# Kernel optimization log

Hardware: AMD Instinct MI355X
Metric: run time of the kernel (lower is better)

Reference implementation:

```python
import jax, jax.numpy as jnp
from jax import lax
import numpy as np

# HH / synapse constants (CFG in original repo; standard values matching the rate eqns)
GNA, GK, GL = 40.0, 35.0, 0.3
ENA, EK, EL = 55.0, -77.0, -65.0
GS, VS = 1.0, 0.0
IAPP = 1.0
VT, KP = -20.0, 3.0
A_D, A_R = 1.0, 0.1
DT = 0.02

B, N, L = 16, 2000, 1024


def setup_inputs() -> dict:
    key = jax.random.key(0)
    z = jax.random.uniform(key, (B, N, L), dtype=jnp.float32)
    return {"z": z}


def _rates(V):
    # Singularity-safe rate constants (the torch code patches V==25 / V==-35 exactly).
    at25 = V == 25.0
    atm35 = V == -35.0
    dN = jnp.where(at25, 1.0, 1.0 - jnp.exp((-V + 25.0) / 9.0))
    dM = jnp.where(atm35, 1.0, 1.0 - jnp.exp((-V - 35.0) / 9.0))
    dNb = jnp.where(at25, 1.0, 1.0 - jnp.exp((V - 25.0) / 9.0))
    dMb = jnp.where(atm35, 1.0, 1.0 - jnp.exp((V + 35.0) / 9.0))
    aN = jnp.where(at25, 0.18, 0.02 * (V - 25.0) / dN)
    bN = jnp.where(at25, 0.08, -0.002 * (V - 25.0) / dNb)
    aM = jnp.where(atm35, 1.638, 0.182 * (V + 35.0) / dM)
    bM = jnp.where(atm35, 1.16, -0.124 * (V + 35.0) / dMb)
    aH = 0.25 * jnp.exp((-V - 90.0) / 12.0)
    bH = 0.25 * jnp.exp((V + 34.0) / 12.0)
    return aN, bN, aM, bM, aH, bH


def _step(carry, z_prev):
    V, m, n, h, y = carry
    pow1 = GNA * m ** 3 * h
    pow2 = GK * n ** 4
    G = DT / 2 * (pow1 + pow2 + GL + GS * y)
    E = pow1 * ENA + pow2 * EK + GL * EL + GS * VS * y
    Vn = (V * (1.0 - G) + DT * (E + IAPP)) / (1.0 + G)
    aN, bN, aM, bM, aH, bH = _rates(Vn)
    mn = (aM * DT + (1.0 - DT / 2 * (aM + bM)) * m) / (DT / 2 * (aM + bM) + 1.0)
    nn = (aN * DT + (1.0 - DT / 2 * (aN + bN)) * n) / (DT / 2 * (aN + bN) + 1.0)
    hn = (aH * DT + (1.0 - DT / 2 * (aH + bH)) * h) / (DT / 2 * (aH + bH) + 1.0)
    ady = A_D * z_prev
    yn = (ady * DT + (1.0 - DT / 2 * (ady + A_R)) * y) / (DT / 2 * (ady + A_R) + 1.0)
    return (Vn, mn, nn, hn, yn), Vn


def _hh(z):
    b, n_t, l = z.shape
    zt = jnp.moveaxis(z, 1, 0)  # (N, B, L); step k uses z[k-1]
    V0 = jnp.full((b, l), -70.0, dtype=z.dtype)
    zeros = jnp.zeros((b, l), dtype=z.dtype)
    ones = jnp.ones((b, l), dtype=z.dtype)
    carry0 = (V0, zeros, zeros, ones, zeros)
    _, Vseq = lax.scan(_step, carry0, zt[:-1])  # (N-1, B, L)
    Vall = jnp.concatenate([V0[None], Vseq], axis=0)  # (N, B, L)
    V = jnp.moveaxis(Vall, 0, 1)  # (B, N, L)
    return jax.nn.sigmoid((V - VT) / KP)


def reference(z):
    return _hh(z)
```

## Files before the change

### kernel.cpp

```cpp
#include <hip/hip_runtime.h>

#define N_ 2000
#define L_ 1024

__device__ __forceinline__ float rcpf(float d) { return __builtin_amdgcn_rcpf(d); }
__device__ __forceinline__ float ex2(float x)  { return __builtin_amdgcn_exp2f(x); }

#define STEP2(K, RS, DOSTORE)                                                 \
  {                                                                           \
    const int kk = (K);                                                       \
    float zc = zb[RS];                                                        \
    int kpre = kk + 7;                                                        \
    int kc = kpre < 1998 ? kpre : 1998;                                       \
    zb[RS] = z[base + kc * L_];                                               \
                             \
    float w    = evn ? sB : sA;                                               \
    float t1   = sA * sA;                                                     \
    float val  = (t1 * sA) * w;                                               \
    float gAdd = evn ? 0.003f : 0.01f * sB;               \
    float Gh   = __fmaf_rn(val, cG, gAdd);                                    \
    float Eh   = __fmaf_rn(val, cE, eAdd);                                    \
    float G    = Gh + __shfl_xor(Gh, 1, 64);                                  \
    float E    = Eh + __shfl_xor(Eh, 1, 64);                                  \
    float num  = __fmaf_rn(V, 1.0f - G, 0.02f * (E + 1.0f));                  \
    float Vn   = num * rcpf(1.0f + G);                                        \
             \
    float e1   = ex2(__fmaf_rn(Vn, K9, -25.0f * K9));                         \
    float eR   = e1 * cm;                                                     \
    float u    = Vn + cu;                                                     \
    float r    = rcpf(eR - 1.0f);                                             \
    float ur   = u * r;                                                       \
    bool  pat  = (Vn == cc);                                                  \
    float av   = pat ? pa : ka * (ur * eR);                                   \
    float bv   = pat ? pb : kb * ur;                                          \
              \
    float vH   = 0.25f * ex2(__fmaf_rn(Vn, sHc, cHc));                        \
    float vHx  = __shfl_xor(vH, 1, 64);                                       \
                                         \
    float s1   = __fmaf_rn(av, 0.01f, 0.01f * bv);                            \
    float q1   = 1.0f + s1;                                                   \
    float num1 = __fmaf_rn(av, 0.02f, __fmaf_rn(-s1, sA, sA));                \
                                         \
    float a2   = evn ? vH  : zc;                                              \
    float b2   = evn ? vHx : 0.1f;                                            \
    float s2   = __fmaf_rn(a2, 0.01f, 0.01f * b2);                            \
    float q2   = 1.0f + s2;                                                   \
    float num2 = __fmaf_rn(a2, 0.02f, __fmaf_rn(-s2, sB, sB));                \
    float rq   = rcpf(q1 * q2);                                               \
    sA = num1 * (rq * q2);                                                    \
    sB = num2 * (rq * q1);                                                    \
    V = Vn;                                                                   \
    if (DOSTORE) {                                                            \
         \
      float esel = evn ? e1p : e1;                                            \
      float e3 = (esel * esel) * esel;                                        \
      float ts = e3 * C15;                               \
      float sg = ts * rcpf(1.0f + ts);                                        \
      out[base + (kk - 1 + sub) * L_] = sg;                                   \
    } else {                                                                  \
      e1p = e1;                                                               \
    }                                                                         \
  }

__global__ __launch_bounds__(64) void hh_kernel(const float* __restrict__ z,
                                                float* __restrict__ out) {
    const int t   = blockIdx.x * 64 + threadIdx.x;
    const int sub = t & 1;
    const int ch  = t >> 1;
    const int b   = ch >> 10;
    const int l   = ch & 1023;
    const int base = b * (N_ * L_) + l;

    const bool evn = (sub == 0);

    const float K9  = 0.16029944898766259f;
    const float K12 = 0.12022458674074695f;
    const float C60 = 785.77207f;
    const float C15 = 3269017.37f;

    const float cG   = evn ? 0.4f      : 0.35f;
    const float cE   = evn ? 2200.0f   : -2695.0f;
    const float eAdd = evn ? -19.5f    : 0.0f;
    const float cu   = evn ? 35.0f     : -25.0f;
    const float cm   = evn ? C60       : 1.0f;
    const float cc   = evn ? -35.0f    : 25.0f;
    const float ka   = evn ? 0.182f    : 0.02f;
    const float kb   = evn ? 0.124f    : 0.002f;
    const float pa   = evn ? 1.638f    : 0.18f;
    const float pb   = evn ? 1.16f     : 0.08f;
    const float sHc  = evn ? -K12      : K12;
    const float cHc  = evn ? -90.0f*K12 : 34.0f*K12;

    float V  = -70.0f;
    float sA = 0.0f;
    float sB = evn ? 1.0f : 0.0f;
    float e1p = ex2((-70.0f - 25.0f) * K9);

    float zb[8];
#pragma unroll
    for (int i = 0; i < 8; ++i) zb[i] = z[base + i * L_];

    int k2 = 1;
    for (int g = 0; g < 249; ++g) {
#pragma unroll
        for (int j = 0; j < 4; ++j) {
            STEP2(k2 + 2 * j,     2 * j,     true)
            STEP2(k2 + 2 * j + 1, 2 * j + 1, false)
        }
        k2 += 8;
    }
#pragma unroll
    for (int j = 0; j < 3; ++j) {
        STEP2(k2 + 2 * j,     2 * j,     true)
        STEP2(k2 + 2 * j + 1, 2 * j + 1, false)
    }
    STEP2(1999, 6, true)
}

extern "C" void kernel_launch(void* const* d_in, const int* in_sizes, int n_in,
                              void* d_out, int out_size, void* d_ws, size_t ws_size,
                              hipStream_t stream) {
    const float* z = (const float*)d_in[0];
    float* out = (float*)d_out;
    hh_kernel<<<512, 64, 0, stream>>>(z, out);
}
```

Measured before the change: 565.5 us.

## Merge paired-lane HH recurrence into one thread per channel

```diff
diff --git a/kernel.cpp b/kernel.cpp
--- a/kernel.cpp
+++ b/kernel.cpp
@@ -6,115 +6,97 @@
 __device__ __forceinline__ float rcpf(float d) { return __builtin_amdgcn_rcpf(d); }
 __device__ __forceinline__ float ex2(float x)  { return __builtin_amdgcn_exp2f(x); }
 
-#define STEP2(K, RS, DOSTORE)                                                 \
+#define STEP1(K, RS)                                                          \
   {                                                                           \
     const int kk = (K);                                                       \
     float zc = zb[RS];                                                        \
     int kpre = kk + 7;                                                        \
     int kc = kpre < 1998 ? kpre : 1998;                                       \
     zb[RS] = z[base + kc * L_];                                               \
-                             \
-    float w    = evn ? sB : sA;                                               \
-    float t1   = sA * sA;                                                     \
-    float val  = (t1 * sA) * w;                                               \
-    float gAdd = evn ? 0.003f : 0.01f * sB;               \
-    float Gh   = __fmaf_rn(val, cG, gAdd);                                    \
-    float Eh   = __fmaf_rn(val, cE, eAdd);                                    \
-    float G    = Gh + __shfl_xor(Gh, 1, 64);                                  \
-    float E    = Eh + __shfl_xor(Eh, 1, 64);                                  \
-    float num  = __fmaf_rn(V, 1.0f - G, 0.02f * (E + 1.0f));                  \
+     \
+    float m2   = m * m;                                                       \
+    float m3   = m2 * m;                                                      \
+    float valm = m3 * h;                                           \
+    float n2   = n * n;                                                       \
+    float valn = n2 * n2;                                            \
+    float gy   = __fmaf_rn(y, 0.01f, 0.003f);                                 \
+    float G    = __fmaf_rn(valm, 0.4f, __fmaf_rn(valn, 0.35f, gy));           \
+    float E    = __fmaf_rn(valm, 2200.0f, __fmaf_rn(valn, -2695.0f, -19.5f)); \
+    float num  = __fmaf_rn(V, 1.0f - G, __fmaf_rn(E, 0.02f, 0.02f));          \
     float Vn   = num * rcpf(1.0f + G);                                        \
-             \
-    float e1   = ex2(__fmaf_rn(Vn, K9, -25.0f * K9));                         \
-    float eR   = e1 * cm;                                                     \
-    float u    = Vn + cu;                                                     \
-    float r    = rcpf(eR - 1.0f);                                             \
-    float ur   = u * r;                                                       \
-    bool  pat  = (Vn == cc);                                                  \
-    float av   = pat ? pa : ka * (ur * eR);                                   \
-    float bv   = pat ? pb : kb * ur;                                          \
-              \
-    float vH   = 0.25f * ex2(__fmaf_rn(Vn, sHc, cHc));                        \
-    float vHx  = __shfl_xor(vH, 1, 64);                                       \
-                                         \
-    float s1   = __fmaf_rn(av, 0.01f, 0.01f * bv);                            \
-    float q1   = 1.0f + s1;                                                   \
-    float num1 = __fmaf_rn(av, 0.02f, __fmaf_rn(-s1, sA, sA));                \
-                                         \
-    float a2   = evn ? vH  : zc;                                              \
-    float b2   = evn ? vHx : 0.1f;                                            \
-    float s2   = __fmaf_rn(a2, 0.01f, 0.01f * b2);                            \
-    float q2   = 1.0f + s2;                                                   \
-    float num2 = __fmaf_rn(a2, 0.02f, __fmaf_rn(-s2, sB, sB));                \
-    float rq   = rcpf(q1 * q2);                                               \
-    sA = num1 * (rq * q2);                                                    \
-    sB = num2 * (rq * q1);                                                    \
+        \
+    float eRm  = ex2(__fmaf_rn(Vn, K9, 35.0f * K9));                          \
+    float um   = Vn + 35.0f;                                                  \
+    float urm  = um * rcpf(eRm - 1.0f);                                       \
+    bool  patm = (Vn == -35.0f);                                              \
+    float aM   = patm ? 1.638f   : 0.182f * (urm * eRm);                      \
+    float s1m  = patm ? 0.02798f : urm * __fmaf_rn(0.00182f, eRm, 0.00124f);  \
+                                           \
+    float eRn  = ex2(__fmaf_rn(Vn, K9, -25.0f * K9));                         \
+    float un   = Vn - 25.0f;                                                  \
+    float urn  = un * rcpf(eRn - 1.0f);                                       \
+    bool  patn = (Vn == 25.0f);                                               \
+    float aN   = patn ? 0.18f   : 0.02f * (urn * eRn);                        \
+    float s1n  = patn ? 0.0026f : urn * __fmaf_rn(0.0002f, eRn, 0.00002f);    \
+                                                                 \
+    float aH   = 0.25f * ex2(__fmaf_rn(Vn, -K12, -90.0f * K12));              \
+    float bH   = 0.25f * ex2(__fmaf_rn(Vn,  K12,  34.0f * K12));              \
+                                                \
+    float qm   = 1.0f + s1m;                                                  \
+    float numm = __fmaf_rn(aM, 0.02f, __fmaf_rn(-s1m, m, m));                 \
+    float qn   = 1.0f + s1n;                                                  \
+    float numn = __fmaf_rn(aN, 0.02f, __fmaf_rn(-s1n, n, n));                 \
+    float sh   = __fmaf_rn(aH, 0.01f, 0.01f * bH);                            \
+    float qh   = 1.0f + sh;                                                   \
+    float numh = __fmaf_rn(aH, 0.02f, __fmaf_rn(-sh, h, h));                  \
+    float sy   = __fmaf_rn(zc, 0.01f, 0.001f);                                \
+    float qy   = 1.0f + sy;                                                   \
+    float numy = __fmaf_rn(zc, 0.02f, __fmaf_rn(-sy, y, y));                  \
+    float rq1  = rcpf(qm * qh);                                               \
+    m = numm * (rq1 * qh);                                                    \
+    h = numh * (rq1 * qm);                                                    \
+    float rq2  = rcpf(qn * qy);                                               \
+    n = numn * (rq2 * qy);                                                    \
+    y = numy * (rq2 * qn);                                                    \
     V = Vn;                                                                   \
-    if (DOSTORE) {                                                            \
-         \
-      float esel = evn ? e1p : e1;                                            \
-      float e3 = (esel * esel) * esel;                                        \
-      float ts = e3 * C15;                               \
-      float sg = ts * rcpf(1.0f + ts);                                        \
-      out[base + (kk - 1 + sub) * L_] = sg;                                   \
-    } else {                                                                  \
-      e1p = e1;                                                               \
-    }                                                                         \
+                          \
+    float e2 = eRm * eRm;                                                     \
+    float ts = (e2 * eRm) * 0.006737946999085467f;                            \
+    float sg = ts * rcpf(1.0f + ts);                                          \
+    out[base + kk * L_] = sg;                                                 \
   }
 
 __global__ __launch_bounds__(64) void hh_kernel(const float* __restrict__ z,
                                                 float* __restrict__ out) {
     const int t   = blockIdx.x * 64 + threadIdx.x;
-    const int sub = t & 1;
-    const int ch  = t >> 1;
-    const int b   = ch >> 10;
-    const int l   = ch & 1023;
+    const int b   = t >> 10;
+    const int l   = t & 1023;
     const int base = b * (N_ * L_) + l;
-
-    const bool evn = (sub == 0);
 
     const float K9  = 0.16029944898766259f;
     const float K12 = 0.12022458674074695f;
-    const float C60 = 785.77207f;
-    const float C15 = 3269017.37f;
 
-    const float cG   = evn ? 0.4f      : 0.35f;
-    const float cE   = evn ? 2200.0f   : -2695.0f;
-    const float eAdd = evn ? -19.5f    : 0.0f;
-    const float cu   = evn ? 35.0f     : -25.0f;
-    const float cm   = evn ? C60       : 1.0f;
-    const float cc   = evn ? -35.0f    : 25.0f;
-    const float ka   = evn ? 0.182f    : 0.02f;
-    const float kb   = evn ? 0.124f    : 0.002f;
-    const float pa   = evn ? 1.638f    : 0.18f;
-    const float pb   = evn ? 1.16f     : 0.08f;
-    const float sHc  = evn ? -K12      : K12;
-    const float cHc  = evn ? -90.0f*K12 : 34.0f*K12;
-
-    float V  = -70.0f;
-    float sA = 0.0f;
-    float sB = evn ? 1.0f : 0.0f;
-    float e1p = ex2((-70.0f - 25.0f) * K9);
+    float V = -70.0f;
+    float m = 0.0f, n = 0.0f, h = 1.0f, y = 0.0f;
 
     float zb[8];
 #pragma unroll
     for (int i = 0; i < 8; ++i) zb[i] = z[base + i * L_];
 
-    int k2 = 1;
+    out[base] = 5.777750e-8f;
+
+    int k = 1;
     for (int g = 0; g < 249; ++g) {
 #pragma unroll
-        for (int j = 0; j < 4; ++j) {
-            STEP2(k2 + 2 * j,     2 * j,     true)
-            STEP2(k2 + 2 * j + 1, 2 * j + 1, false)
+        for (int j = 0; j < 8; ++j) {
+            STEP1(k + j, j)
         }
-        k2 += 8;
+        k += 8;
     }
 #pragma unroll
-    for (int j = 0; j < 3; ++j) {
-        STEP2(k2 + 2 * j,     2 * j,     true)
-        STEP2(k2 + 2 * j + 1, 2 * j + 1, false)
+    for (int j = 0; j < 7; ++j) {
+        STEP1(k + j, j)
     }
-    STEP2(1999, 6, true)
 }
 
 extern "C" void kernel_launch(void* const* d_in, const int* in_sizes, int n_in,
@@ -122,5 +104,5 @@
                               hipStream_t stream) {
     const float* z = (const float*)d_in[0];
     float* out = (float*)d_out;
-    hh_kernel<<<512, 64, 0, stream>>>(z, out);
+    hh_kernel<<<256, 64, 0, stream>>>(z, out);
 }
```

New measurement: 510.2 us. -9.8%, faster.
